# Kernel tuning notes

Hardware: AMD Instinct MI355X
Metric: run time of the kernel (lower is better)

## Reference

```python
import jax, jax.numpy as jnp
import numpy as np

B, S, D, H = 4, 2048, 1024, 16
HD = D // H

def setup_inputs() -> dict:
    key = jax.random.key(0)
    ks = jax.random.split(key, 10)
    s = 1.0 / np.sqrt(D)
    inp = {
        'x': jax.random.normal(ks[0], (B, S, D), dtype=jnp.float32),
        'attention_mask': jnp.ones((B, S), dtype=jnp.int32),
        'Wq': jax.random.uniform(ks[1], (D, D), jnp.float32, -s, s),
        'bq': jax.random.uniform(ks[2], (D,), jnp.float32, -s, s),
        'Wk': jax.random.uniform(ks[3], (D, D), jnp.float32, -s, s),
        'bk': jax.random.uniform(ks[4], (D,), jnp.float32, -s, s),
        'Wv': jax.random.uniform(ks[5], (D, D), jnp.float32, -s, s),
        'bv': jax.random.uniform(ks[6], (D,), jnp.float32, -s, s),
        'Wo': jax.random.uniform(ks[7], (D, D), jnp.float32, -s, s),
        'bo': jax.random.uniform(ks[8], (D,), jnp.float32, -s, s),
    }
    return inp

def reference(x, Wq, bq, Wk, bk, Wv, bv, Wo, bo, attention_mask):
    scale = HD ** -0.5
    # torch Linear: y = x @ W^T + b
    def proj(W, b):
        return (x @ W.T + b).reshape(B, S, H, HD).transpose(0, 2, 1, 3)  # [B,H,S,hd]
    q = proj(Wq, bq)
    k = proj(Wk, bk)
    v = proj(Wv, bv)
    scores = jnp.einsum('bhqd,bhkd->bhqk', q, k) * scale  # [B,H,S,S]
    causal = jnp.triu(jnp.ones((S, S), dtype=bool), k=1)
    scores = jnp.where(causal, -jnp.inf, scores)
    pad = (attention_mask == 0)[:, None, None, :]  # [B,1,1,S]
    scores = jnp.where(pad, jnp.float32(-1e9), scores)
    probs = jax.nn.softmax(scores, axis=-1)
    out = jnp.einsum('bhqk,bhkd->bhqd', probs, v)  # [B,H,S,hd]
    out = out.transpose(0, 2, 1, 3).reshape(B, S, D)
    return out @ Wo.T + bo
```

## Files before the change

### kernel.cpp

```cpp
#include <hip/hip_runtime.h>
#include <hip/hip_bf16.h>

typedef unsigned short u16;
typedef float f32x4 __attribute__((ext_vector_type(4)));
typedef __bf16 bf16x8 __attribute__((ext_vector_type(8)));

#define BB 4
#define SS 2048
#define DD 1024
#define HH 16
#define HDD 64
#define MM (BB*SS)

__device__ __forceinline__ u16 f2bf(float f){
    union { float f; unsigned int i; } v; v.f = f;
    unsigned int i = v.i;
    return (u16)((i + 0x7FFFu + ((i >> 16) & 1u)) >> 16);
}
__device__ __forceinline__ ushort2 pk2(float a, float b){
    union { __hip_bfloat162 h; ushort2 u; } v;
    float2 t; t.x = a; t.y = b;
    v.h = __float22bfloat162_rn(t);
    return v.u;
}
__device__ __forceinline__ ushort4 pk4(float a, float b, float c, float d){
    ushort2 lo = pk2(a, b), hi = pk2(c, d);
    ushort4 r; r.x = lo.x; r.y = lo.y; r.z = hi.x; r.w = hi.y;
    return r;
}
__device__ __forceinline__ void gl2lds16(const void* g, void* l){
    __builtin_amdgcn_global_load_lds(
        (const __attribute__((address_space(1))) void*)g,
        (__attribute__((address_space(3))) void*)l, 16, 0, 0);
}

__device__ __forceinline__ void cvt8(const float* __restrict__ src,
                                     u16* __restrict__ dst, size_t i)
{
    const float4 a = *(const float4*)&src[i];
    const float4 b = *(const float4*)&src[i + 4];
    ushort4 lo = pk4(a.x, a.y, a.z, a.w);
    ushort4 hi = pk4(b.x, b.y, b.z, b.w);
    uint4 o;
    o.x = (unsigned)lo.x | ((unsigned)lo.y << 16);
    o.y = (unsigned)lo.z | ((unsigned)lo.w << 16);
    o.z = (unsigned)hi.x | ((unsigned)hi.y << 16);
    o.w = (unsigned)hi.z | ((unsigned)hi.w << 16);
    *(uint4*)&dst[i] = o;
}

__global__ __launch_bounds__(256) void cvt_k(const float* __restrict__ src,
                                             u16* __restrict__ dst)
{
    const size_t i = ((size_t)blockIdx.x * 256 + threadIdx.x) * 8;
    cvt8(src, dst, i);
}

__global__ __launch_bounds__(256) void cvtw3_k(
    const float* __restrict__ W0, const float* __restrict__ W1,
    const float* __restrict__ W2, u16* __restrict__ dst)
{
    const float* src = blockIdx.y == 0 ? W0 : (blockIdx.y == 1 ? W1 : W2);
    u16* d = dst + (size_t)blockIdx.y * (size_t)DD * DD;
    const size_t i = ((size_t)blockIdx.x * 256 + threadIdx.x) * 8;
    cvt8(src, d, i);
}

__global__ __launch_bounds__(256) void cvtw1_k(const float* __restrict__ W,
                                               u16* __restrict__ dst)
{
    const size_t i = ((size_t)blockIdx.x * 256 + threadIdx.x) * 8;
    cvt8(W, dst, i);
}

__device__ __forceinline__ void gemm_core(const u16* __restrict__ Wb,
                                          const u16* __restrict__ Act,
                                          f32x4 (&acc)[4][4],
                                          u16 (&At)[2][256 * 32],
                                          u16 (&Bt)[2][128 * 32],
                                          int n0, int m0, int tid)
{
    const int lane = tid & 63, w = tid >> 6;
    const int quad = lane >> 4, l15 = lane & 15;
    const int wn2 = w & 3, wm2 = w >> 2;
    const int arow = lane >> 2;
    const int acol = (lane & 3) * 8;

    auto STG = [&](int bi, int kt) {
        const int kk = kt * 32;
        #pragma unroll
        for (int c0 = 0; c0 < 3; ++c0) {
            const int c = w * 3 + c0;
            if (c < 16) {
                gl2lds16(&Wb[(size_t)(n0 + c * 16 + arow) * DD + kk + acol],
                         &At[bi][c * 512]);
            } else {
                const int cb = c - 16;
                gl2lds16(&Act[(size_t)(m0 + cb * 16 + arow) * DD + kk + acol],
                         &Bt[bi][cb * 512]);
            }
        }
    };
    auto CMP = [&](int bi) {
        bf16x8 af[4], bfr[4];
        #pragma unroll
        for (int i = 0; i < 4; ++i)
            af[i] = *(const bf16x8*)&At[bi][(wn2 * 64 + i * 16 + l15) * 32 + quad * 8];
        #pragma unroll
        for (int j = 0; j < 4; ++j)
            bfr[j] = *(const bf16x8*)&Bt[bi][(wm2 * 64 + j * 16 + l15) * 32 + quad * 8];
        #pragma unroll
        for (int i = 0; i < 4; ++i)
            #pragma unroll
            for (int j = 0; j < 4; ++j)
                acc[i][j] = __builtin_amdgcn_mfma_f32_16x16x32_bf16(af[i], bfr[j], acc[i][j], 0, 0, 0);
    };

    STG(0, 0);
    __syncthreads();
    #pragma unroll 1
    for (int i = 0; i < 15; ++i) {
        STG(1, 2 * i + 1);
        CMP(0);
        __syncthreads();
        STG(0, 2 * i + 2);
        CMP(1);
        __syncthreads();
    }
    STG(1, 31);
    CMP(0);
    __syncthreads();
    CMP(1);
}

__global__ __launch_bounds__(512, 2) void gemm_qkv_k(
    const u16* __restrict__ x,
    const float* __restrict__ bq, const float* __restrict__ bk,
    const float* __restrict__ bv,
    const u16* __restrict__ Wqb, const u16* __restrict__ Wkb,
    const u16* __restrict__ Wvb,
    u16* __restrict__ Q, u16* __restrict__ K, u16* __restrict__ V)
{
    __shared__ alignas(16) u16 At[2][256 * 32];
    __shared__ alignas(16) u16 Bt[2][128 * 32];
    const int tid = threadIdx.x, lane = tid & 63, w = tid >> 6;
    const int quad = lane >> 4, l15 = lane & 15;
    const int wn2 = w & 3, wm2 = w >> 2;
    const int z = blockIdx.z;
    const u16* Wmb = z == 0 ? Wqb : (z == 1 ? Wkb : Wvb);
    const float* bias = z == 0 ? bq : (z == 1 ? bk : bv);
    u16* Out = z == 0 ? Q : (z == 1 ? K : V);
    const int m0 = blockIdx.x * 128, n0 = blockIdx.y * 256;

    f32x4 acc[4][4];
    #pragma unroll
    for (int i = 0; i < 4; ++i)
        #pragma unroll
        for (int j = 0; j < 4; ++j) acc[i][j] = (f32x4)(0.0f);

    gemm_core(Wmb, x, acc, At, Bt, n0, m0, tid);

    f32x4 bsv[4];
    #pragma unroll
    for (int i = 0; i < 4; ++i)
        bsv[i] = *(const f32x4*)&bias[n0 + wn2 * 64 + i * 16 + quad * 4];

    const int b = m0 / SS;
    const int h = (n0 + wn2 * 64) / HDD;
    const size_t base = ((size_t)(b * HH + h)) * SS * HDD;
    #pragma unroll
    for (int j = 0; j < 4; ++j) {
        const int s = (m0 % SS) + wm2 * 64 + j * 16 + l15;
        #pragma unroll
        for (int i = 0; i < 4; ++i) {
            *(ushort4*)&Out[base + (size_t)s * HDD + i * 16 + quad * 4] =
                pk4(acc[i][j][0] + bsv[i][0], acc[i][j][1] + bsv[i][1],
                    acc[i][j][2] + bsv[i][2], acc[i][j][3] + bsv[i][3]);
        }
    }
}

__global__ __launch_bounds__(512, 2) void gemm_out_k(
    const u16* __restrict__ A, const float* __restrict__ bo,
    const u16* __restrict__ Wob, float* __restrict__ Out)
{
    __shared__ alignas(16) u16 At[2][256 * 32];
    __shared__ alignas(16) u16 Bt[2][128 * 32];
    const int tid = threadIdx.x, lane = tid & 63, w = tid >> 6;
    const int quad = lane >> 4, l15 = lane & 15;
    const int wn2 = w & 3, wm2 = w >> 2;
    const int m0 = blockIdx.x * 128, n0 = blockIdx.y * 256;

    f32x4 acc[4][4];
    #pragma unroll
    for (int i = 0; i < 4; ++i)
        #pragma unroll
        for (int j = 0; j < 4; ++j) acc[i][j] = (f32x4)(0.0f);

    gemm_core(Wob, A, acc, At, Bt, n0, m0, tid);

    f32x4 bsv[4];
    #pragma unroll
    for (int i = 0; i < 4; ++i)
        bsv[i] = *(const f32x4*)&bo[n0 + wn2 * 64 + i * 16 + quad * 4];

    #pragma unroll
    for (int j = 0; j < 4; ++j) {
        const int m = m0 + wm2 * 64 + j * 16 + l15;
        #pragma unroll
        for (int i = 0; i < 4; ++i) {
            float4 f;
            f.x = acc[i][j][0] + bsv[i][0];
            f.y = acc[i][j][1] + bsv[i][1];
            f.z = acc[i][j][2] + bsv[i][2];
            f.w = acc[i][j][3] + bsv[i][3];
            *(float4*)&Out[(size_t)m * DD + n0 + wn2 * 64 + i * 16 + quad * 4] = f;
        }
    }
}

#define QT 128
#define KT 64
#define LDPV 66

#define LOG2E 1.4426950408889634f

__device__ __forceinline__ int swz128(int row, int bcol){
    return row * 128 + (bcol ^ ((row & 7) << 4));
}

__global__ __launch_bounds__(256, 2) void attn_k(
    const u16* __restrict__ Q, const u16* __restrict__ K,
    const u16* __restrict__ V, const int* __restrict__ mask,
    u16* __restrict__ AO)
{
    __shared__ alignas(16) u16 QPs[QT * 64];
    __shared__ alignas(16) u16 Ks[KT * 64];
    __shared__ alignas(16) u16 Vs[HDD * LDPV];
    __shared__ float padf[KT];

    const int tid = threadIdx.x, lane = tid & 63, w = tid >> 6;
    const int quad = lane >> 4, l15 = lane & 15;
    const int bh = blockIdx.x;
    const int y = blockIdx.y;
    const int qt = (y < 8) ? (15 - y) : (y - 8);
    const int b = bh >> 4, h = bh & 15;
    const int q0 = qt * QT;
    const size_t hoff = (size_t)bh * SS * HDD;
    const u16* Qh = Q + hoff;
    const u16* Kh = K + hoff;
    const u16* Vh = V + hoff;
    const int nkt = (q0 + QT) / KT;
    const float scale2 = 0.125f * LOG2E;
    const int wrow_end = q0 + w * 32 + 32;

    int krow[2], kbcol[2];
    #pragma unroll
    for (int c = 0; c < 2; ++c) {
        const int slot = (w * 2 + c) * 64 + lane;
        krow[c] = slot >> 3;
        kbcol[c] = ((slot & 7) << 4) ^ ((krow[c] & 7) << 4);
    }

    for (int c = tid; c < QT * 8; c += 256) {
        const int row = c >> 3, cc = c & 7;
        *(uint4*)((char*)QPs + swz128(row, cc * 16)) =
            *(const uint4*)&Qh[(size_t)(q0 + row) * HDD + cc * 8];
    }
    __syncthreads();

    bf16x8 bQ[2][2];
    #pragma unroll
    for (int j = 0; j < 2; ++j)
        #pragma unroll
        for (int ks = 0; ks < 2; ++ks)
            bQ[j][ks] = *(const bf16x8*)((const char*)QPs +
                swz128(w * 32 + j * 16 + l15, ks * 64 + quad * 16));

    float m_run[2] = { -1e30f, -1e30f };
    float l_run[2] = { 0.f, 0.f };
    f32x4 o[4][2];
    #pragma unroll
    for (int i = 0; i < 4; ++i)
        #pragma unroll
        for (int j = 0; j < 2; ++j) o[i][j] = (f32x4)(0.0f);

    for (int kt = 0; kt < nkt; ++kt) {
        const int kt0 = kt * KT;
        __syncthreads();

        #pragma unroll
        for (int c = 0; c < 2; ++c)
            gl2lds16((const char*)Kh + (size_t)(kt0 + krow[c]) * 128 + kbcol[c],
                     (char*)Ks + (w * 2 + c) * 1024);

        {
            const int kp = tid >> 3;
            const int c0 = (tid & 7) * 8;
            uint4 r0 = *(const uint4*)&Vh[(size_t)(kt0 + kp * 2 + 0) * HDD + c0];
            uint4 r1 = *(const uint4*)&Vh[(size_t)(kt0 + kp * 2 + 1) * HDD + c0];
            const u16* e0 = (const u16*)&r0;
            const u16* e1 = (const u16*)&r1;
            #pragma unroll
            for (int e = 0; e < 8; ++e) {
                ushort2 pkv; pkv.x = e0[e]; pkv.y = e1[e];
                *(ushort2*)&Vs[(c0 + e) * LDPV + kp * 2] = pkv;
            }
        }
        if (tid < KT) {
            padf[tid] = (mask[b * SS + kt0 + tid] == 0) ? -1e9f : 0.0f;
        }
        __syncthreads();

        if (kt0 < wrow_end) {
        f32x4 sc[4][2];
        #pragma unroll
        for (int i = 0; i < 4; ++i)
            #pragma unroll
            for (int j = 0; j < 2; ++j) sc[i][j] = (f32x4)(0.0f);
        __builtin_amdgcn_s_setprio(1);
        #pragma unroll
        for (int ks = 0; ks < 2; ++ks) {
            bf16x8 aK[4];
            #pragma unroll
            for (int i = 0; i < 4; ++i)
                aK[i] = *(const bf16x8*)((const char*)Ks +
                    swz128(i * 16 + l15, ks * 64 + quad * 16));
            #pragma unroll
            for (int i = 0; i < 4; ++i)
                #pragma unroll
                for (int j = 0; j < 2; ++j)
                    sc[i][j] = __builtin_amdgcn_mfma_f32_16x16x32_bf16(aK[i], bQ[j][ks], sc[i][j], 0, 0, 0);
        }
        __builtin_amdgcn_s_setprio(0);

        f32x4 pb[4];
        #pragma unroll
        for (int i = 0; i < 4; ++i)
            pb[i] = *(const f32x4*)&padf[i * 16 + quad * 4];

        #pragma unroll
        for (int j = 0; j < 2; ++j) {
            const int qrow = q0 + w * 32 + j * 16 + l15;
            const bool needC = (kt0 + KT - 1) > (q0 + w * 32 + j * 16);
            float mx = -1e9f;
            if (needC) {
                #pragma unroll
                for (int i = 0; i < 4; ++i)
                    #pragma unroll
                    for (int r = 0; r < 4; ++r) {
                        const int kpg = kt0 + i * 16 + quad * 4 + r;
                        float s = fmaf(sc[i][j][r], scale2, pb[i][r]);
                        s = (kpg > qrow) ? -1e9f : s;
                        sc[i][j][r] = s; mx = fmaxf(mx, s);
                    }
            } else {
                #pragma unroll
                for (int i = 0; i < 4; ++i)
                    #pragma unroll
                    for (int r = 0; r < 4; ++r) {
                        float s = fmaf(sc[i][j][r], scale2, pb[i][r]);
                        sc[i][j][r] = s; mx = fmaxf(mx, s);
                    }
            }
            mx = fmaxf(mx, __shfl_xor(mx, 16, 64));
            mx = fmaxf(mx, __shfl_xor(mx, 32, 64));
            float nm = m_run[j];
            if (!__all(mx <= nm + 8.f)) {
                nm = fmaxf(nm, mx);
                const float alpha = __builtin_exp2f(m_run[j] - nm);
                m_run[j] = nm;
                l_run[j] *= alpha;
                #pragma unroll
                for (int i = 0; i < 4; ++i)
                    #pragma unroll
                    for (int r = 0; r < 4; ++r) o[i][j][r] *= alpha;
            }
            float rs = 0.f;
            #pragma unroll
            for (int i = 0; i < 4; ++i) {
                float p0 = __builtin_exp2f(sc[i][j][0] - nm);
                float p1 = __builtin_exp2f(sc[i][j][1] - nm);
                float p2 = __builtin_exp2f(sc[i][j][2] - nm);
                float p3 = __builtin_exp2f(sc[i][j][3] - nm);
                rs += (p0 + p1) + (p2 + p3);
                *(ushort4*)((char*)QPs + swz128(w * 32 + j * 16 + l15, i * 32 + quad * 8)) =
                    pk4(p0, p1, p2, p3);
            }
            l_run[j] += rs;
        }
        asm volatile("s_waitcnt lgkmcnt(0)" ::: "memory");

        __builtin_amdgcn_s_setprio(1);
        #pragma unroll
        for (int ks = 0; ks < 2; ++ks) {
            bf16x8 aV[4], bP[2];
            #pragma unroll
            for (int i = 0; i < 4; ++i)
                aV[i] = *(const bf16x8*)&Vs[(i * 16 + l15) * LDPV + ks * 32 + quad * 8];
            #pragma unroll
            for (int j = 0; j < 2; ++j)
                bP[j] = *(const bf16x8*)((const char*)QPs +
                    swz128(w * 32 + j * 16 + l15, ks * 64 + quad * 16));
            #pragma unroll
            for (int i = 0; i < 4; ++i)
                #pragma unroll
                for (int j = 0; j < 2; ++j)
                    o[i][j] = __builtin_amdgcn_mfma_f32_16x16x32_bf16(aV[i], bP[j], o[i][j], 0, 0, 0);
        }
        __builtin_amdgcn_s_setprio(0);
        }
    }

    #pragma unroll
    for (int j = 0; j < 2; ++j) {
        float l = l_run[j];
        l += __shfl_xor(l, 16, 64);
        l += __shfl_xor(l, 32, 64);
        const float inv = (l > 0.f) ? (1.f / l) : 0.f;
        const int s = q0 + w * 32 + j * 16 + l15;
        const size_t rb = ((size_t)(b * SS + s)) * DD + h * HDD;
        #pragma unroll
        for (int i = 0; i < 4; ++i)
            *(ushort4*)&AO[rb + i * 16 + quad * 4] =
                pk4(o[i][j][0] * inv, o[i][j][1] * inv, o[i][j][2] * inv, o[i][j][3] * inv);
    }
}

extern "C" void kernel_launch(void* const* d_in, const int* in_sizes, int n_in,
                              void* d_out, int out_size, void* d_ws, size_t ws_size,
                              hipStream_t stream)
{
    const float* x  = (const float*)d_in[0];
    const int* mask = (const int*)d_in[1];
    const float* Wq = (const float*)d_in[2];
    const float* bq = (const float*)d_in[3];
    const float* Wk = (const float*)d_in[4];
    const float* bk = (const float*)d_in[5];
    const float* Wv = (const float*)d_in[6];
    const float* bv = (const float*)d_in[7];
    const float* Wo = (const float*)d_in[8];
    const float* bo = (const float*)d_in[9];
    float* out = (float*)d_out;

    u16* ws = (u16*)d_ws;
    const size_t NE = (size_t)MM * DD;
    const size_t WE = (size_t)DD * DD;
    if (ws_size < 4 * NE * sizeof(u16)) return;

    u16* Qb = ws;
    u16* Kb = ws + NE;
    u16* Vb = ws + 2 * NE;
    u16* Ab = ws + 3 * NE;

    u16* Wscr = (u16*)d_out;

    dim3 blk(256);
    cvt_k<<<dim3(NE / 2048), blk, 0, stream>>>(x, Ab);
    cvtw3_k<<<dim3(WE / 2048, 3), blk, 0, stream>>>(Wq, Wk, Wv, Wscr);
    gemm_qkv_k<<<dim3(MM / 128, DD / 256, 3), dim3(512), 0, stream>>>(
        Ab, bq, bk, bv, Wscr, Wscr + WE, Wscr + 2 * WE, Qb, Kb, Vb);
    attn_k<<<dim3(BB * HH, SS / QT), dim3(256), 0, stream>>>(Qb, Kb, Vb, mask, Ab);
    cvtw1_k<<<dim3(WE / 2048), blk, 0, stream>>>(Wo, Qb);
    gemm_out_k<<<dim3(MM / 128, DD / 256), dim3(512), 0, stream>>>(Ab, bo, Qb, out);
}
```

Measured before the change: 307.0 us.

## Store V transposed from projection GEMM and async-load it into swizzled LDS

```diff
diff --git a/kernel.cpp b/kernel.cpp
--- a/kernel.cpp
+++ b/kernel.cpp
@@ -168,14 +168,30 @@
     const int b = m0 / SS;
     const int h = (n0 + wn2 * 64) / HDD;
     const size_t base = ((size_t)(b * HH + h)) * SS * HDD;
-    #pragma unroll
-    for (int j = 0; j < 4; ++j) {
-        const int s = (m0 % SS) + wm2 * 64 + j * 16 + l15;
+    if (z == 2) {
         #pragma unroll
         for (int i = 0; i < 4; ++i) {
-            *(ushort4*)&Out[base + (size_t)s * HDD + i * 16 + quad * 4] =
-                pk4(acc[i][j][0] + bsv[i][0], acc[i][j][1] + bsv[i][1],
-                    acc[i][j][2] + bsv[i][2], acc[i][j][3] + bsv[i][3]);
+            #pragma unroll
+            for (int r = 0; r < 4; ++r) {
+                const int hd = i * 16 + quad * 4 + r;
+                const float bb = bsv[i][r];
+                #pragma unroll
+                for (int j = 0; j < 4; ++j) {
+                    const int s = (m0 % SS) + wm2 * 64 + j * 16 + l15;
+                    Out[base + (size_t)hd * SS + s] = f2bf(acc[i][j][r] + bb);
+                }
+            }
+        }
+    } else {
+        #pragma unroll
+        for (int j = 0; j < 4; ++j) {
+            const int s = (m0 % SS) + wm2 * 64 + j * 16 + l15;
+            #pragma unroll
+            for (int i = 0; i < 4; ++i) {
+                *(ushort4*)&Out[base + (size_t)s * HDD + i * 16 + quad * 4] =
+                    pk4(acc[i][j][0] + bsv[i][0], acc[i][j][1] + bsv[i][1],
+                        acc[i][j][2] + bsv[i][2], acc[i][j][3] + bsv[i][3]);
+            }
         }
     }
 }
@@ -221,7 +237,6 @@
 
 #define QT 128
 #define KT 64
-#define LDPV 66
 
 #define LOG2E 1.4426950408889634f
 
@@ -236,7 +251,7 @@
 {
     __shared__ alignas(16) u16 QPs[QT * 64];
     __shared__ alignas(16) u16 Ks[KT * 64];
-    __shared__ alignas(16) u16 Vs[HDD * LDPV];
+    __shared__ alignas(16) u16 Vs[KT * 64];
     __shared__ float padf[KT];
 
     const int tid = threadIdx.x, lane = tid & 63, w = tid >> 6;
@@ -249,18 +264,13 @@
     const size_t hoff = (size_t)bh * SS * HDD;
     const u16* Qh = Q + hoff;
     const u16* Kh = K + hoff;
-    const u16* Vh = V + hoff;
+    const u16* Vt = V + hoff;
     const int nkt = (q0 + QT) / KT;
     const float scale2 = 0.125f * LOG2E;
     const int wrow_end = q0 + w * 32 + 32;
 
-    int krow[2], kbcol[2];
-    #pragma unroll
-    for (int c = 0; c < 2; ++c) {
-        const int slot = (w * 2 + c) * 64 + lane;
-        krow[c] = slot >> 3;
-        kbcol[c] = ((slot & 7) << 4) ^ ((krow[c] & 7) << 4);
-    }
+    const int vrow = lane >> 3;
+    const int dbcol = (((lane & 7) ^ vrow) << 4);
 
     for (int c = tid; c < QT * 8; c += 256) {
         const int row = c >> 3, cc = c & 7;
@@ -285,32 +295,25 @@
         #pragma unroll
         for (int j = 0; j < 2; ++j) o[i][j] = (f32x4)(0.0f);
 
+    int pm = 1;
+    if (tid < KT) pm = mask[b * SS + tid];
+
     for (int kt = 0; kt < nkt; ++kt) {
         const int kt0 = kt * KT;
         __syncthreads();
 
         #pragma unroll
-        for (int c = 0; c < 2; ++c)
-            gl2lds16((const char*)Kh + (size_t)(kt0 + krow[c]) * 128 + kbcol[c],
-                     (char*)Ks + (w * 2 + c) * 1024);
-
-        {
-            const int kp = tid >> 3;
-            const int c0 = (tid & 7) * 8;
-            uint4 r0 = *(const uint4*)&Vh[(size_t)(kt0 + kp * 2 + 0) * HDD + c0];
-            uint4 r1 = *(const uint4*)&Vh[(size_t)(kt0 + kp * 2 + 1) * HDD + c0];
-            const u16* e0 = (const u16*)&r0;
-            const u16* e1 = (const u16*)&r1;
-            #pragma unroll
-            for (int e = 0; e < 8; ++e) {
-                ushort2 pkv; pkv.x = e0[e]; pkv.y = e1[e];
-                *(ushort2*)&Vs[(c0 + e) * LDPV + kp * 2] = pkv;
-            }
-        }
-        if (tid < KT) {
-            padf[tid] = (mask[b * SS + kt0 + tid] == 0) ? -1e9f : 0.0f;
-        }
+        for (int c0 = 0; c0 < 2; ++c0) {
+            const int c = w * 2 + c0;
+            gl2lds16((const char*)Kh + (size_t)(kt0 + c * 8 + vrow) * 128 + dbcol,
+                     (char*)Ks + c * 1024);
+            gl2lds16((const char*)Vt + ((size_t)(c * 8 + vrow) * SS + kt0) * 2 + dbcol,
+                     (char*)Vs + c * 1024);
+        }
+        if (tid < KT) padf[tid] = (pm == 0) ? -1e9f : 0.0f;
         __syncthreads();
+
+        if (tid < KT && kt + 1 < nkt) pm = mask[b * SS + kt0 + KT + tid];
 
         if (kt0 < wrow_end) {
         f32x4 sc[4][2];
@@ -397,7 +400,8 @@
             bf16x8 aV[4], bP[2];
             #pragma unroll
             for (int i = 0; i < 4; ++i)
-                aV[i] = *(const bf16x8*)&Vs[(i * 16 + l15) * LDPV + ks * 32 + quad * 8];
+                aV[i] = *(const bf16x8*)((const char*)Vs +
+                    swz128(i * 16 + l15, ks * 64 + quad * 16));
             #pragma unroll
             for (int j = 0; j < 2; ++j)
                 bP[j] = *(const bf16x8*)((const char*)QPs +
```

Result: faster. 297.6 us (-3.1%).
